# Kernel tuning notes

Measured on AMD Instinct MI355X. Metric: run time of the kernel, lower is better.

## Reference

```python
import jax, jax.numpy as jnp
import numpy as np

N_HEADS = 16

def setup_inputs() -> dict:
    key = jax.random.key(0)
    ks = jax.random.split(key, 5)
    D = 2048
    x = jax.random.normal(ks[0], (2, 2048, D), dtype=jnp.float32)
    scale = 1.0 / np.sqrt(D)
    Wq = jax.random.normal(ks[1], (D, D), dtype=jnp.float32) * scale
    Wk = jax.random.normal(ks[2], (D, D), dtype=jnp.float32) * scale
    Wv = jax.random.normal(ks[3], (D, D), dtype=jnp.float32) * scale
    Wo = jax.random.normal(ks[4], (D, D), dtype=jnp.float32) * scale
    return {"x": x, "Wq": Wq, "Wk": Wk, "Wv": Wv, "Wo": Wo}


def reference(x, Wq, Wk, Wv, Wo):
    # Causal multi-head attention. The original module computes it one query
    # position at a time (recompute loop) but the math is standard causal MHA:
    # query pos attends to key positions 0..pos.
    B, S, D = x.shape
    H = N_HEADS
    hd = D // H
    def split_heads(t):
        return t.reshape(B, S, H, hd).transpose(0, 2, 1, 3)  # (B,H,S,hd)
    q = split_heads(x @ Wq.T)
    k = split_heads(x @ Wk.T)
    v = split_heads(x @ Wv.T)
    scores = jnp.einsum('bhqd,bhkd->bhqk', q, k) / jnp.sqrt(jnp.asarray(hd, x.dtype))
    causal = jnp.tril(jnp.ones((S, S), dtype=bool))  # (S,S), True where allowed
    scores = jnp.where(causal[None, None], scores, jnp.asarray(-jnp.inf, scores.dtype))
    attn = jax.nn.softmax(scores, axis=-1)
    out = jnp.einsum('bhqk,bhkd->bhqd', attn, v)
    out = out.transpose(0, 2, 1, 3).reshape(B, S, D)
    return out @ Wo.T
```

## Files before the change

kernel.cpp:

```cpp
#include <hip/hip_runtime.h>
#include <stdint.h>

#define DD 2048
#define SS 2048
#define NB 2
#define NH 16
#define HDIM 128
#define MM (NB*SS)

typedef __attribute__((ext_vector_type(8))) short bf16x8;
typedef __attribute__((ext_vector_type(4))) float f32x4;
typedef __attribute__((ext_vector_type(4))) ushort u16x4;

__device__ __forceinline__ float fast_exp2(float x) {
  return __builtin_amdgcn_exp2f(x);
}

__device__ __forceinline__ ushort f2bf(float f) {
  union { float f; uint32_t u; } v; v.f = f;
  uint32_t u = v.u;
  return (ushort)((u + 0x7fffu + ((u >> 16) & 1u)) >> 16);
}

__device__ __forceinline__ void gld_lds16(const ushort* g, ushort* l) {
  __builtin_amdgcn_global_load_lds(
      (const __attribute__((address_space(1))) void*)g,
      (__attribute__((address_space(3))) void*)l, 16, 0, 0);
}

__global__ __launch_bounds__(256) void cvt_all(
    const float* __restrict__ x, const float* __restrict__ wq,
    const float* __restrict__ wk, const float* __restrict__ wv,
    const float* __restrict__ wo, ushort* __restrict__ dst)
{
  int i8 = blockIdx.x * 256 + threadIdx.x;
  const int X8 = MM * DD / 8;
  const int W8 = DD * DD / 8;
  const float* src; int off;
  if (i8 < X8)            { src = x;  off = i8; }
  else if (i8 < X8 +   W8){ src = wq; off = i8 - X8; }
  else if (i8 < X8 + 2*W8){ src = wk; off = i8 - (X8 +   W8); }
  else if (i8 < X8 + 3*W8){ src = wv; off = i8 - (X8 + 2*W8); }
  else                    { src = wo; off = i8 - (X8 + 3*W8); }
  const float4* p = (const float4*)src;
  float4 a = p[(long)off*2], b = p[(long)off*2 + 1];
  bf16x8 o;
  o[0]=(short)f2bf(a.x); o[1]=(short)f2bf(a.y); o[2]=(short)f2bf(a.z); o[3]=(short)f2bf(a.w);
  o[4]=(short)f2bf(b.x); o[5]=(short)f2bf(b.y); o[6]=(short)f2bf(b.z); o[7]=(short)f2bf(b.w);
  *(bf16x8*)(dst + (long)i8*8) = o;
}

template<int MODE>
__global__ __launch_bounds__(256, 2) void gemm_tri(
    const ushort* __restrict__ A, const ushort* __restrict__ Bt,
    ushort* __restrict__ Qo, ushort* __restrict__ Ko, ushort* __restrict__ Vt,
    float* __restrict__ Cf)
{
  __shared__ ushort lds[3 * 12288];
  const int t = threadIdx.x;
  const int bid = blockIdx.x;
  const int xcd = bid & 7, local = bid >> 3;
  const int NBX = (MODE == 0) ? 6 : 2;
  const int bm = local / NBX;
  const int bn = xcd * NBX + (local - bm * NBX);
  const int lane = t & 63, w = t >> 6;
  const int wr = w >> 1, wcn = w & 1;
  const int lr = lane & 15, lg = lane >> 4;

  int aoff[4], boff[2];
#pragma unroll
  for (int i = 0; i < 4; ++i) {
    int p = i*256 + t, ln = p >> 3, sr = (p & 7) ^ (ln & 7);
    aoff[i] = (2*ln + (sr >> 2)) * DD + (sr & 3) * 8;
  }
#pragma unroll
  for (int i = 0; i < 2; ++i) {
    int p = i*256 + t, ln = p >> 3, sr = (p & 7) ^ (ln & 7);
    boff[i] = (2*ln + (sr >> 2)) * DD + (sr & 3) * 8;
  }
  const ushort* Ab = A  + (long)(bm*256) * DD;
  const ushort* Bb = Bt + (long)(bn*128) * DD;

#define STG_A01(KT, BUF) do { const ushort* g_ = Ab + (KT)*32;             \
    ushort* l_ = lds + (BUF)*12288;                                        \
    gld_lds16(g_ + aoff[0], l_ + t*8);                                     \
    gld_lds16(g_ + aoff[1], l_ + (256 + t)*8); } while (0)
#define STG_A23(KT, BUF) do { const ushort* g_ = Ab + (KT)*32;             \
    ushort* l_ = lds + (BUF)*12288;                                        \
    gld_lds16(g_ + aoff[2], l_ + (512 + t)*8);                             \
    gld_lds16(g_ + aoff[3], l_ + (768 + t)*8); } while (0)
#define STG_B(KT, BUF)   do { const ushort* g_ = Bb + (KT)*32;             \
    ushort* l_ = lds + (BUF)*12288 + 8192;                                 \
    gld_lds16(g_ + boff[0], l_ + t*8);                                     \
    gld_lds16(g_ + boff[1], l_ + (256 + t)*8); } while (0)
#define LDA(dst, m) { int r_ = wr*128 + (m)*16 + lr; int ln_ = r_ >> 1;    \
    int sl_ = (lg + ((r_ & 1) << 2)) ^ (ln_ & 7);                          \
    (dst) = *(const bf16x8*)(cb + ln_*128 + sl_*16); }
#define LDB(dst, n) { int r_ = wcn*64 + (n)*16 + lr; int ln_ = r_ >> 1;    \
    int sl_ = (lg + ((r_ & 1) << 2)) ^ (ln_ & 7);                          \
    (dst) = *(const bf16x8*)(cb + 16384 + ln_*128 + sl_*16); }
#define MFMA42(AV, BV, MB, NB_) do {                                       \
    __builtin_amdgcn_s_setprio(1);                                         \
    _Pragma("unroll") for (int m = 0; m < 4; ++m)                          \
    _Pragma("unroll") for (int n = 0; n < 2; ++n)                          \
      acc[(MB)+m][(NB_)+n] = __builtin_amdgcn_mfma_f32_16x16x32_bf16(      \
          AV[m], BV[n], acc[(MB)+m][(NB_)+n], 0, 0, 0);                    \
    __builtin_amdgcn_s_setprio(0); } while (0)
#define SB  __builtin_amdgcn_sched_barrier(0)
#define BAR __builtin_amdgcn_s_barrier()
#define LGKM0 asm volatile("s_waitcnt lgkmcnt(0)" ::: "memory")

  f32x4 acc[8][4] = {};
  const int T = DD / 32;

  STG_A01(0, 0); STG_A23(0, 0); STG_B(0, 0);
  STG_A01(1, 1); STG_A23(1, 1); STG_B(1, 1);
  asm volatile("s_waitcnt vmcnt(6)" ::: "memory");
  SB; BAR; SB;

  for (int kt = 0; kt < T; ++kt) {
    const char* cb = (const char*)lds + (kt % 3) * 24576;
    const int bs = (kt + 2) % 3;
    const bool st = (kt + 2 < T);
    bf16x8 a03[4], a47[4], b01[2], b23[2];
    LDA(a03[0],0); LDA(a03[1],1); LDA(a03[2],2); LDA(a03[3],3);
    LDB(b01[0],0); LDB(b01[1],1);
    if (st) STG_A01(kt+2, bs);
    SB; BAR; LGKM0; SB;
    MFMA42(a03, b01, 0, 0);
    SB; BAR; SB;
    LDA(a47[0],4); LDA(a47[1],5); LDA(a47[2],6); LDA(a47[3],7);
    if (st) STG_A23(kt+2, bs);
    SB; BAR; LGKM0; SB;
    MFMA42(a47, b01, 4, 0);
    SB; BAR; SB;
    LDB(b23[0],2); LDB(b23[1],3);
    if (st) STG_B(kt+2, bs);
    SB; BAR; LGKM0; SB;
    MFMA42(a03, b23, 0, 2);
    SB; BAR; SB;
    if (st)              { asm volatile("s_waitcnt vmcnt(6)" ::: "memory"); }
    else if (kt + 1 < T) { asm volatile("s_waitcnt vmcnt(0)" ::: "memory"); }
    SB; BAR; SB;
    MFMA42(a47, b23, 4, 2);
    SB; BAR; SB;
  }
#undef STG_A01
#undef STG_A23
#undef STG_B
#undef LDA
#undef LDB
#undef MFMA42
#undef SB
#undef BAR
#undef LGKM0

  const int crb = bm*256 + wr*128 + lg*4;
  if (MODE == 0) {
    const int region = bn >> 4;
    const int ccb = (bn & 15)*128 + wcn*64 + lr;
    if (region < 2) {
      const float scale = (region == 0) ? (0.08838834764831845f * 1.4426950408889634f) : 1.0f;
      ushort* C = (region == 0) ? Qo : Ko;
#pragma unroll
      for (int m = 0; m < 8; ++m)
#pragma unroll
        for (int n = 0; n < 4; ++n)
#pragma unroll
          for (int j = 0; j < 4; ++j)
            C[(long)(crb + m*16 + j) * DD + (ccb + n*16)] = f2bf(acc[m][n][j] * scale);
    } else {
#pragma unroll
      for (int m = 0; m < 8; ++m) {
        int sg = crb + m*16;
        int b2 = sg >> 11, s2 = sg & 2047;
#pragma unroll
        for (int n = 0; n < 4; ++n) {
          int colv = ccb + n*16;
          int h2 = colv >> 7, d2 = colv & 127;
          u16x4 pk;
          pk[0] = f2bf(acc[m][n][0]); pk[1] = f2bf(acc[m][n][1]);
          pk[2] = f2bf(acc[m][n][2]); pk[3] = f2bf(acc[m][n][3]);
          *(u16x4*)(Vt + ((long)((b2*NH + h2)*HDIM + d2)) * SS + s2) = pk;
        }
      }
    }
  } else {
    const int ccb = bn*128 + wcn*64 + lr;
#pragma unroll
    for (int m = 0; m < 8; ++m)
#pragma unroll
      for (int n = 0; n < 4; ++n)
#pragma unroll
        for (int j = 0; j < 4; ++j)
          Cf[(long)(crb + m*16 + j) * DD + (ccb + n*16)] = acc[m][n][j];
  }
}

__global__ __launch_bounds__(512, 2) void attn_fwd(
    const ushort* __restrict__ Qb, const ushort* __restrict__ Kb,
    const ushort* __restrict__ Vtg, ushort* __restrict__ Ob)
{
  __shared__ ushort Ks[2][128*128];
  __shared__ ushort Vs[2][128*128];
  __shared__ ushort Ps[8*16*68];

  const int bid = blockIdx.x;
  const int p = bid >> 5;
  const int bh = bid & 31;
  const int b = bh >> 4, h = bh & 15;
  const int t = threadIdx.x;
  const int lane = t & 63;
  const int wq = t >> 6;
  const int lr = lane & 15, lg = lane >> 4;

  int koff[4], voff[4];
#pragma unroll
  for (int i = 0; i < 4; ++i) {
    int c = i*512 + t;
    int kr = c >> 4, kc = c & 15;
    koff[i] = kr*DD + ((kc ^ (kr & 7)) * 8);
    voff[i] = kr*SS + ((kc ^ (kr & 7)) * 8);
  }
  const ushort* Kg = Kb + (long)(b * SS) * DD + h * HDIM;
  const ushort* Vg = Vtg + (long)(bh * HDIM) * SS;

#define STAGE(KT, BUF) do {                                     \
    const ushort* kg_ = Kg + (long)(KT) * 128 * DD;             \
    const ushort* vg_ = Vg + (KT) * 128;                        \
    _Pragma("unroll") for (int i_ = 0; i_ < 4; ++i_) {          \
      gld_lds16(kg_ + koff[i_], &Ks[BUF][i_*4096 + t*8]);       \
      gld_lds16(vg_ + voff[i_], &Vs[BUF][i_*4096 + t*8]);       \
    } } while (0)

  ushort* myP = Ps + wq * (16*68);
  const int n0 = p + 1;
  const int TOT = 17;

  STAGE(0, 0);
  __syncthreads();

  int u = 0;
  for (int half = 0; half < 2; ++half) {
    const int qt = half ? (15 - p) : p;
    const int qbase = qt * 128;
    const long rowQ = (long)(b * SS + qbase + wq * 16);
    const int ntile = qt + 1;
    const int qminw = qbase + wq*16;

    bf16x8 qf[4];
#pragma unroll
    for (int c = 0; c < 4; ++c)
      qf[c] = *(const bf16x8*)(Qb + (rowQ + lr) * DD + h*HDIM + c*32 + lg*8);

    f32x4 accO[8] = {};
    float mrow[4], lrow[4];
#pragma unroll
    for (int j = 0; j < 4; ++j) { mrow[j] = -1e30f; lrow[j] = 0.f; }

    for (int kt = 0; kt < ntile; ++kt, ++u) {
      const int k0 = kt * 128;
      const int cur = u & 1;
      if (u + 1 < TOT) {
        const int un = u + 1;
        const int ktn = (un < n0) ? un : un - n0;
        STAGE(ktn, cur ^ 1);
      }

      const ushort* Kc = Ks[cur];
      const ushort* Vc = Vs[cur];
      f32x4 sc[8] = {};
      __builtin_amdgcn_s_setprio(1);
#pragma unroll
      for (int n = 0; n < 8; ++n) {
        int r = n*16 + lr;
        int swz = (r & 7) << 4;
#pragma unroll
        for (int c = 0; c < 4; ++c) {
          bf16x8 kf = *(const bf16x8*)((const char*)Kc + ((r*256 + c*64 + lg*16) ^ swz));
          sc[n] = __builtin_amdgcn_mfma_f32_16x16x32_bf16(qf[c], kf, sc[n], 0,0,0);
        }
      }
      __builtin_amdgcn_s_setprio(0);
      if (kt == ntile - 1) {
#pragma unroll
        for (int n = 0; n < 8; ++n)
#pragma unroll
          for (int j = 0; j < 4; ++j) {
            int kpos = k0 + n*16 + lr;
            int qpos = qminw + lg*4 + j;
            if (kpos > qpos) sc[n][j] = -1e30f;
          }
      }
      float al[4];
#pragma unroll
      for (int j = 0; j < 4; ++j) {
        float tm = fmaxf(fmaxf(fmaxf(sc[0][j], sc[1][j]), fmaxf(sc[2][j], sc[3][j])),
                         fmaxf(fmaxf(sc[4][j], sc[5][j]), fmaxf(sc[6][j], sc[7][j])));
#pragma unroll
        for (int off = 1; off < 16; off <<= 1) tm = fmaxf(tm, __shfl_xor(tm, off));
        float mn = fmaxf(mrow[j], tm);
        float a = fast_exp2(mrow[j] - mn);
        mrow[j] = mn;
        float ts = 0.f;
#pragma unroll
        for (int n = 0; n < 8; ++n) {
          float pv = fast_exp2(sc[n][j] - mn);
          sc[n][j] = pv; ts += pv;
        }
#pragma unroll
        for (int off = 1; off < 16; off <<= 1) ts += __shfl_xor(ts, off);
        lrow[j] = lrow[j] * a + ts;
        al[j] = a;
      }
#pragma unroll
      for (int dg = 0; dg < 8; ++dg) {
        f32x4 v = accO[dg];
        v[0] *= al[0]; v[1] *= al[1]; v[2] *= al[2]; v[3] *= al[3];
        accO[dg] = v;
      }
#pragma unroll
      for (int hh = 0; hh < 2; ++hh) {
#pragma unroll
        for (int n2 = 0; n2 < 4; ++n2)
#pragma unroll
          for (int j = 0; j < 4; ++j)
            myP[(lg*4 + j)*68 + n2*16 + lr] = f2bf(sc[hh*4 + n2][j]);
        bf16x8 pa0 = *(const bf16x8*)(myP + lr*68 + lg*8);
        bf16x8 pa1 = *(const bf16x8*)(myP + lr*68 + 32 + lg*8);
        __builtin_amdgcn_s_setprio(1);
#pragma unroll
        for (int dg = 0; dg < 8; ++dg) {
          int d = dg*16 + lr;
          int vswz = (d & 7) << 4;
          const char* vrow = (const char*)Vc + d*256 + hh*128;
          bf16x8 v0 = *(const bf16x8*)((const char*)Vc + ((d*256 + hh*128 + lg*16) ^ vswz));
          bf16x8 v1 = *(const bf16x8*)((const char*)Vc + ((d*256 + hh*128 + 64 + lg*16) ^ vswz));
          (void)vrow;
          accO[dg] = __builtin_amdgcn_mfma_f32_16x16x32_bf16(pa0, v0, accO[dg], 0,0,0);
          accO[dg] = __builtin_amdgcn_mfma_f32_16x16x32_bf16(pa1, v1, accO[dg], 0,0,0);
        }
        __builtin_amdgcn_s_setprio(0);
      }
      __syncthreads();
    }

    float inv[4];
#pragma unroll
    for (int j = 0; j < 4; ++j) inv[j] = 1.0f / lrow[j];
    ushort* Og = Ob + rowQ * DD + h * HDIM;
#pragma unroll
    for (int dg = 0; dg < 8; ++dg)
#pragma unroll
      for (int j = 0; j < 4; ++j)
        Og[(long)(lg*4 + j) * DD + dg*16 + lr] = f2bf(accO[dg][j] * inv[j]);
  }
#undef STAGE
}

extern "C" void kernel_launch(void* const* d_in, const int* in_sizes, int n_in,
                              void* d_out, int out_size, void* d_ws, size_t ws_size,
                              hipStream_t stream) {
  const float* x  = (const float*)d_in[0];
  const float* Wq = (const float*)d_in[1];
  const float* Wk = (const float*)d_in[2];
  const float* Wv = (const float*)d_in[3];
  const float* Wo = (const float*)d_in[4];

  ushort* ws  = (ushort*)d_ws;
  ushort* xb  = ws;
  ushort* wqb = ws  + (long)MM*DD;
  ushort* wkb = wqb + (long)DD*DD;
  ushort* wvb = wkb + (long)DD*DD;
  ushort* wob = wvb + (long)DD*DD;
  ushort* Qb  = wob + (long)DD*DD;
  ushort* Kb  = Qb  + (long)MM*DD;
  ushort* Vtg = Kb  + (long)MM*DD;
  (void)wkb; (void)wvb;

  const int CVT_BLOCKS = (MM*DD + 4*DD*DD) / 8 / 256;
  cvt_all<<<CVT_BLOCKS, 256, 0, stream>>>(x, Wq, Wk, Wv, Wo, ws);

  gemm_tri<0><<<768, 256, 0, stream>>>(xb, wqb, Qb, Kb, Vtg, nullptr);

  attn_fwd<<<256, 512, 0, stream>>>(Qb, Kb, Vtg, xb);

  gemm_tri<1><<<256, 256, 0, stream>>>(xb, wob, nullptr, nullptr, nullptr,
                                       (float*)d_out);
}
```

Before: 251.2 us.

## Use 128x128 tile GEMM for output projection and lazy softmax rescaling

The output projection GEMM moves from a 256x128 tile launched on 256 blocks to a dedicated 128x128 tile kernel on 512 blocks with three blocks per CU, so the 256-CU device gets better occupancy. In attention, the running max and accumulator rescale are updated only when some row's new max exceeds the stored max by more than 8 (log2 units), skipping the exp and multiplies over the output accumulator otherwise. The lazy rescale lets unnormalized probabilities reach up to 2^8, which slightly raises overflow and precision risk in bf16 P values. It also adds a wave-wide vote and a branch to each tile.

```diff
diff --git a/kernel.cpp b/kernel.cpp
--- a/kernel.cpp
+++ b/kernel.cpp
@@ -50,17 +50,15 @@
   *(bf16x8*)(dst + (long)i8*8) = o;
 }
 
-template<int MODE>
-__global__ __launch_bounds__(256, 2) void gemm_tri(
+__global__ __launch_bounds__(256, 2) void gemm_qkv(
     const ushort* __restrict__ A, const ushort* __restrict__ Bt,
-    ushort* __restrict__ Qo, ushort* __restrict__ Ko, ushort* __restrict__ Vt,
-    float* __restrict__ Cf)
+    ushort* __restrict__ Qo, ushort* __restrict__ Ko, ushort* __restrict__ Vt)
 {
   __shared__ ushort lds[3 * 12288];
   const int t = threadIdx.x;
   const int bid = blockIdx.x;
   const int xcd = bid & 7, local = bid >> 3;
-  const int NBX = (MODE == 0) ? 6 : 2;
+  const int NBX = 6;
   const int bm = local / NBX;
   const int bn = xcd * NBX + (local - bm * NBX);
   const int lane = t & 63, w = t >> 6;
@@ -151,50 +149,136 @@
 #undef LDA
 #undef LDB
 #undef MFMA42
+
+  const int crb = bm*256 + wr*128 + lg*4;
+  const int region = bn >> 4;
+  const int ccb = (bn & 15)*128 + wcn*64 + lr;
+  if (region < 2) {
+    const float scale = (region == 0) ? (0.08838834764831845f * 1.4426950408889634f) : 1.0f;
+    ushort* C = (region == 0) ? Qo : Ko;
+#pragma unroll
+    for (int m = 0; m < 8; ++m)
+#pragma unroll
+      for (int n = 0; n < 4; ++n)
+#pragma unroll
+        for (int j = 0; j < 4; ++j)
+          C[(long)(crb + m*16 + j) * DD + (ccb + n*16)] = f2bf(acc[m][n][j] * scale);
+  } else {
+#pragma unroll
+    for (int m = 0; m < 8; ++m) {
+      int sg = crb + m*16;
+      int b2 = sg >> 11, s2 = sg & 2047;
+#pragma unroll
+      for (int n = 0; n < 4; ++n) {
+        int colv = ccb + n*16;
+        int h2 = colv >> 7, d2 = colv & 127;
+        u16x4 pk;
+        pk[0] = f2bf(acc[m][n][0]); pk[1] = f2bf(acc[m][n][1]);
+        pk[2] = f2bf(acc[m][n][2]); pk[3] = f2bf(acc[m][n][3]);
+        *(u16x4*)(Vt + ((long)((b2*NH + h2)*HDIM + d2)) * SS + s2) = pk;
+      }
+    }
+  }
 #undef SB
 #undef BAR
 #undef LGKM0
-
-  const int crb = bm*256 + wr*128 + lg*4;
-  if (MODE == 0) {
-    const int region = bn >> 4;
-    const int ccb = (bn & 15)*128 + wcn*64 + lr;
-    if (region < 2) {
-      const float scale = (region == 0) ? (0.08838834764831845f * 1.4426950408889634f) : 1.0f;
-      ushort* C = (region == 0) ? Qo : Ko;
-#pragma unroll
-      for (int m = 0; m < 8; ++m)
-#pragma unroll
-        for (int n = 0; n < 4; ++n)
-#pragma unroll
-          for (int j = 0; j < 4; ++j)
-            C[(long)(crb + m*16 + j) * DD + (ccb + n*16)] = f2bf(acc[m][n][j] * scale);
-    } else {
-#pragma unroll
-      for (int m = 0; m < 8; ++m) {
-        int sg = crb + m*16;
-        int b2 = sg >> 11, s2 = sg & 2047;
-#pragma unroll
-        for (int n = 0; n < 4; ++n) {
-          int colv = ccb + n*16;
-          int h2 = colv >> 7, d2 = colv & 127;
-          u16x4 pk;
-          pk[0] = f2bf(acc[m][n][0]); pk[1] = f2bf(acc[m][n][1]);
-          pk[2] = f2bf(acc[m][n][2]); pk[3] = f2bf(acc[m][n][3]);
-          *(u16x4*)(Vt + ((long)((b2*NH + h2)*HDIM + d2)) * SS + s2) = pk;
-        }
-      }
-    }
-  } else {
-    const int ccb = bn*128 + wcn*64 + lr;
-#pragma unroll
-    for (int m = 0; m < 8; ++m)
-#pragma unroll
-      for (int n = 0; n < 4; ++n)
-#pragma unroll
-        for (int j = 0; j < 4; ++j)
-          Cf[(long)(crb + m*16 + j) * DD + (ccb + n*16)] = acc[m][n][j];
-  }
+}
+
+__global__ __launch_bounds__(256, 3) void gemm_o128(
+    const ushort* __restrict__ A, const ushort* __restrict__ Bt,
+    float* __restrict__ Cf)
+{
+  __shared__ ushort lds[3 * 8192];
+  const int t = threadIdx.x;
+  const int bid = blockIdx.x;
+  const int xcd = bid & 7, local = bid >> 3;
+  const int bm = local >> 1;
+  const int bn = xcd * 2 + (local & 1);
+  const int lane = t & 63, w = t >> 6;
+  const int wr = w >> 1, wcn = w & 1;
+  const int lr = lane & 15, lg = lane >> 4;
+
+  int aoff[2], boff[2];
+#pragma unroll
+  for (int i = 0; i < 2; ++i) {
+    int p = i*256 + t, ln = p >> 3, sr = (p & 7) ^ (ln & 7);
+    aoff[i] = (2*ln + (sr >> 2)) * DD + (sr & 3) * 8;
+    boff[i] = aoff[i];
+  }
+  const ushort* Ab = A  + (long)(bm*128) * DD;
+  const ushort* Bb = Bt + (long)(bn*128) * DD;
+
+#define STG_A(KT, BUF) do { const ushort* g_ = Ab + (KT)*32;               \
+    ushort* l_ = lds + (BUF)*8192;                                         \
+    gld_lds16(g_ + aoff[0], l_ + t*8);                                     \
+    gld_lds16(g_ + aoff[1], l_ + (256 + t)*8); } while (0)
+#define STG_B(KT, BUF) do { const ushort* g_ = Bb + (KT)*32;               \
+    ushort* l_ = lds + (BUF)*8192 + 4096;                                  \
+    gld_lds16(g_ + boff[0], l_ + t*8);                                     \
+    gld_lds16(g_ + boff[1], l_ + (256 + t)*8); } while (0)
+#define LDA(dst, m) { int r_ = wr*64 + (m)*16 + lr; int ln_ = r_ >> 1;     \
+    int sl_ = (lg + ((r_ & 1) << 2)) ^ (ln_ & 7);                          \
+    (dst) = *(const bf16x8*)(cb + ln_*128 + sl_*16); }
+#define LDB(dst, n) { int r_ = wcn*64 + (n)*16 + lr; int ln_ = r_ >> 1;    \
+    int sl_ = (lg + ((r_ & 1) << 2)) ^ (ln_ & 7);                          \
+    (dst) = *(const bf16x8*)(cb + 8192 + ln_*128 + sl_*16); }
+#define MFMA8(AV, BV, NB_) do {                                            \
+    __builtin_amdgcn_s_setprio(1);                                         \
+    _Pragma("unroll") for (int m = 0; m < 4; ++m)                          \
+    _Pragma("unroll") for (int n = 0; n < 2; ++n)                          \
+      acc[m][(NB_)+n] = __builtin_amdgcn_mfma_f32_16x16x32_bf16(           \
+          AV[m], BV[n], acc[m][(NB_)+n], 0, 0, 0);                         \
+    __builtin_amdgcn_s_setprio(0); } while (0)
+#define SB  __builtin_amdgcn_sched_barrier(0)
+#define BAR __builtin_amdgcn_s_barrier()
+#define LGKM0 asm volatile("s_waitcnt lgkmcnt(0)" ::: "memory")
+
+  f32x4 acc[4][4] = {};
+  const int T = DD / 32;
+
+  STG_A(0, 0); STG_B(0, 0);
+  STG_A(1, 1); STG_B(1, 1);
+  asm volatile("s_waitcnt vmcnt(4)" ::: "memory");
+  SB; BAR; SB;
+
+  for (int kt = 0; kt < T; ++kt) {
+    const char* cb = (const char*)lds + (kt % 3) * 16384;
+    const int bs = (kt + 2) % 3;
+    const bool st = (kt + 2 < T);
+    bf16x8 a[4], b01[2], b23[2];
+    LDA(a[0],0); LDA(a[1],1); LDA(a[2],2); LDA(a[3],3);
+    LDB(b01[0],0); LDB(b01[1],1);
+    if (st) STG_A(kt+2, bs);
+    SB; BAR; LGKM0; SB;
+    MFMA8(a, b01, 0);
+    SB; BAR; SB;
+    LDB(b23[0],2); LDB(b23[1],3);
+    if (st) STG_B(kt+2, bs);
+    SB; BAR; LGKM0; SB;
+    MFMA8(a, b23, 2);
+    SB;
+    if (st)              { asm volatile("s_waitcnt vmcnt(4)" ::: "memory"); }
+    else if (kt + 1 < T) { asm volatile("s_waitcnt vmcnt(0)" ::: "memory"); }
+    SB; BAR; SB;
+  }
+#undef STG_A
+#undef STG_B
+#undef LDA
+#undef LDB
+#undef MFMA8
+#undef SB
+#undef BAR
+#undef LGKM0
+
+  const int crb = bm*128 + wr*64 + lg*4;
+  const int ccb = bn*128 + wcn*64 + lr;
+#pragma unroll
+  for (int m = 0; m < 4; ++m)
+#pragma unroll
+    for (int n = 0; n < 4; ++n)
+#pragma unroll
+      for (int j = 0; j < 4; ++j)
+        Cf[(long)(crb + m*16 + j) * DD + (ccb + n*16)] = acc[m][n][j];
 }
 
 __global__ __launch_bounds__(512, 2) void attn_fwd(
@@ -292,32 +376,43 @@
             if (kpos > qpos) sc[n][j] = -1e30f;
           }
       }
+      float tm[4]; float gd = -1e30f;
+#pragma unroll
+      for (int j = 0; j < 4; ++j) {
+        float m8 = fmaxf(fmaxf(fmaxf(sc[0][j], sc[1][j]), fmaxf(sc[2][j], sc[3][j])),
+                         fmaxf(fmaxf(sc[4][j], sc[5][j]), fmaxf(sc[6][j], sc[7][j])));
+#pragma unroll
+        for (int off = 1; off < 16; off <<= 1) m8 = fmaxf(m8, __shfl_xor(m8, off));
+        tm[j] = m8;
+        gd = fmaxf(gd, m8 - mrow[j]);
+      }
+      const bool resc = !__all(gd <= 8.0f);
       float al[4];
+      if (resc) {
+#pragma unroll
+        for (int j = 0; j < 4; ++j) {
+          float mn = fmaxf(mrow[j], tm[j]);
+          al[j] = fast_exp2(mrow[j] - mn);
+          mrow[j] = mn;
+        }
+#pragma unroll
+        for (int dg = 0; dg < 8; ++dg) {
+          f32x4 v = accO[dg];
+          v[0] *= al[0]; v[1] *= al[1]; v[2] *= al[2]; v[3] *= al[3];
+          accO[dg] = v;
+        }
+      }
 #pragma unroll
       for (int j = 0; j < 4; ++j) {
-        float tm = fmaxf(fmaxf(fmaxf(sc[0][j], sc[1][j]), fmaxf(sc[2][j], sc[3][j])),
-                         fmaxf(fmaxf(sc[4][j], sc[5][j]), fmaxf(sc[6][j], sc[7][j])));
-#pragma unroll
-        for (int off = 1; off < 16; off <<= 1) tm = fmaxf(tm, __shfl_xor(tm, off));
-        float mn = fmaxf(mrow[j], tm);
-        float a = fast_exp2(mrow[j] - mn);
-        mrow[j] = mn;
         float ts = 0.f;
 #pragma unroll
         for (int n = 0; n < 8; ++n) {
-          float pv = fast_exp2(sc[n][j] - mn);
+          float pv = fast_exp2(sc[n][j] - mrow[j]);
           sc[n][j] = pv; ts += pv;
         }
 #pragma unroll
         for (int off = 1; off < 16; off <<= 1) ts += __shfl_xor(ts, off);
-        lrow[j] = lrow[j] * a + ts;
-        al[j] = a;
-      }
-#pragma unroll
-      for (int dg = 0; dg < 8; ++dg) {
-        f32x4 v = accO[dg];
-        v[0] *= al[0]; v[1] *= al[1]; v[2] *= al[2]; v[3] *= al[3];
-        accO[dg] = v;
+        lrow[j] = (resc ? lrow[j] * al[j] : lrow[j]) + ts;
       }
 #pragma unroll
       for (int hh = 0; hh < 2; ++hh) {
@@ -333,10 +428,8 @@
         for (int dg = 0; dg < 8; ++dg) {
           int d = dg*16 + lr;
           int vswz = (d & 7) << 4;
-          const char* vrow = (const char*)Vc + d*256 + hh*128;
           bf16x8 v0 = *(const bf16x8*)((const char*)Vc + ((d*256 + hh*128 + lg*16) ^ vswz));
           bf16x8 v1 = *(const bf16x8*)((const char*)Vc + ((d*256 + hh*128 + 64 + lg*16) ^ vswz));
-          (void)vrow;
           accO[dg] = __builtin_amdgcn_mfma_f32_16x16x32_bf16(pa0, v0, accO[dg], 0,0,0);
           accO[dg] = __builtin_amdgcn_mfma_f32_16x16x32_bf16(pa1, v1, accO[dg], 0,0,0);
         }
@@ -381,10 +474,9 @@
   const int CVT_BLOCKS = (MM*DD + 4*DD*DD) / 8 / 256;
   cvt_all<<<CVT_BLOCKS, 256, 0, stream>>>(x, Wq, Wk, Wv, Wo, ws);
 
-  gemm_tri<0><<<768, 256, 0, stream>>>(xb, wqb, Qb, Kb, Vtg, nullptr);
+  gemm_qkv<<<768, 256, 0, stream>>>(xb, wqb, Qb, Kb, Vtg);
 
   attn_fwd<<<256, 512, 0, stream>>>(Qb, Kb, Vtg, xb);
 
-  gemm_tri<1><<<256, 256, 0, stream>>>(xb, wob, nullptr, nullptr, nullptr,
-                                       (float*)d_out);
-}
+  gemm_o128<<<512, 256, 0, stream>>>(xb, wob, (float*)d_out);
+}
```

New measurement: 249.5 us. About the same (-0.7%).
